# Kernel optimization log

Measured on AMD Instinct MI355X. Metric: run time of the kernel, lower is better.

The kernel has to match this reference:

```python
import jax, jax.numpy as jnp
import numpy as np

N_EMBD = 1024
N_HEAD = 16
HEAD_DIM = N_EMBD // N_HEAD
B, T = 2, 2048


def setup_inputs() -> dict:
    key = jax.random.key(0)
    k1, k2, k3 = jax.random.split(key, 3)
    s_in = 1.0 / np.sqrt(N_EMBD)
    return {
        "x": jax.random.normal(k1, (B, T, N_EMBD), dtype=jnp.float32),
        "w_qkv": jax.random.normal(k2, (N_EMBD, 3 * N_EMBD), dtype=jnp.float32) * s_in,
        "b_qkv": jnp.zeros((3 * N_EMBD,), dtype=jnp.float32),
        "w_out": jax.random.normal(k3, (N_EMBD, N_EMBD), dtype=jnp.float32) * s_in,
        "b_out": jnp.zeros((N_EMBD,), dtype=jnp.float32),
    }


def reference(x, w_qkv, b_qkv, w_out, b_out):
    b, t, c = x.shape
    qkv = x @ w_qkv + b_qkv  # [B,T,3C]
    q, k, v = jnp.split(qkv, 3, axis=-1)
    # [B,T,C] -> [B,H,T,D]
    reshape = lambda a: a.reshape(b, t, N_HEAD, HEAD_DIM).transpose(0, 2, 1, 3)
    q, k, v = reshape(q), reshape(k), reshape(v)
    scale = 1.0 / jnp.sqrt(jnp.asarray(HEAD_DIM, dtype=x.dtype))
    att = jnp.einsum("bhqd,bhkd->bhqk", q, k) * scale  # [B,H,T,T]
    causal = jnp.tril(jnp.ones((t, t), dtype=bool))
    att = jnp.where(causal, att, jnp.asarray(-jnp.inf, dtype=att.dtype))
    att = jax.nn.softmax(att, axis=-1)
    y = jnp.einsum("bhqk,bhkd->bhqd", att, v)  # [B,H,T,D]
    y = y.transpose(0, 2, 1, 3).reshape(b, t, c)
    return y @ w_out + b_out
```

## Files before the change

### kernel.cpp

```cpp
#include <hip/hip_runtime.h>

typedef unsigned short u16;
typedef __attribute__((ext_vector_type(8))) short s16x8;
typedef __attribute__((ext_vector_type(8))) unsigned short u16x8;
typedef __attribute__((ext_vector_type(4))) unsigned short u16x4;
typedef __attribute__((ext_vector_type(4))) float f32x4;

__device__ __forceinline__ u16 f2bf(float f) {
  unsigned int u = __float_as_uint(f);
  u += 0x7fffu + ((u >> 16) & 1u);
  return (u16)(u >> 16);
}

__device__ __forceinline__ void gload_lds16(const u16* g, u16* l) {
  __builtin_amdgcn_global_load_lds((__attribute__((address_space(1))) void*)(u16*)g,
                                   (__attribute__((address_space(3))) void*)l, 16, 0, 0);
}

__global__ void __launch_bounds__(256) cvt_bf16_kernel(const float* __restrict__ in,
                                                       u16* __restrict__ out) {
  int i = (blockIdx.x * 256 + threadIdx.x) * 8;
  float4 a = *(const float4*)(in + i);
  float4 b = *(const float4*)(in + i + 4);
  u16x8 o;
  o[0] = f2bf(a.x); o[1] = f2bf(a.y); o[2] = f2bf(a.z); o[3] = f2bf(a.w);
  o[4] = f2bf(b.x); o[5] = f2bf(b.y); o[6] = f2bf(b.z); o[7] = f2bf(b.w);
  *(u16x8*)(out + i) = o;
}

__global__ void __launch_bounds__(256) transpose_cvt_kernel(const float* __restrict__ in,
                                                            u16* __restrict__ out,
                                                            int K, int N) {
  __shared__ float tile[32][33];
  int n0 = blockIdx.x * 32, k0 = blockIdx.y * 32;
  int r = threadIdx.x >> 5, c = threadIdx.x & 31;
#pragma unroll
  for (int i = 0; i < 4; ++i)
    tile[r + i * 8][c] = in[(size_t)(k0 + r + i * 8) * N + n0 + c];
  __syncthreads();
#pragma unroll
  for (int i = 0; i < 4; ++i)
    out[(size_t)(n0 + r + i * 8) * K + k0 + c] = f2bf(tile[c][r + i * 8]);
}

__device__ __forceinline__ void gemm_core(const u16* __restrict__ A,
                                          const u16* __restrict__ BT, int K,
                                          int m0, int n0, u16* As, u16* Bs,
                                          f32x4 acc[4][4]) {
  const int tid = threadIdx.x;
  const int lane = tid & 63, wave = tid >> 6;
  const int quad = lane >> 4, l16 = lane & 15;
  const int wm = (wave & 1) << 6, wn = (wave >> 1) << 6;
  const int ob0 = wave * 2048 + lane * 16;
  const int ob1 = ob0 + 1024;
  const int r0 = ob0 >> 6, c0 = (ob0 & 63) >> 1;
  const int r1 = ob1 >> 6, c1 = (ob1 & 63) >> 1;

  for (int k0 = 0; k0 < K; k0 += 32) {
    __syncthreads();
    gload_lds16(&A [(size_t)(m0 + r0) * K + k0 + c0], &As[ob0 >> 1]);
    gload_lds16(&A [(size_t)(m0 + r1) * K + k0 + c1], &As[ob1 >> 1]);
    gload_lds16(&BT[(size_t)(n0 + r0) * K + k0 + c0], &Bs[ob0 >> 1]);
    gload_lds16(&BT[(size_t)(n0 + r1) * K + k0 + c1], &Bs[ob1 >> 1]);
    __syncthreads();
    s16x8 a[4], b[4];
#pragma unroll
    for (int i = 0; i < 4; ++i)
      a[i] = *(const s16x8*)&As[(wm + i * 16 + l16) * 32 + quad * 8];
#pragma unroll
    for (int j = 0; j < 4; ++j)
      b[j] = *(const s16x8*)&Bs[(wn + j * 16 + l16) * 32 + quad * 8];
#pragma unroll
    for (int i = 0; i < 4; ++i)
#pragma unroll
      for (int j = 0; j < 4; ++j)
        acc[i][j] = __builtin_amdgcn_mfma_f32_16x16x32_bf16(a[i], b[j], acc[i][j], 0, 0, 0);
  }
}

__global__ void __launch_bounds__(256) gemm_qkv_kernel(const u16* __restrict__ xbf,
                                                       const u16* __restrict__ wT,
                                                       const float* __restrict__ bias,
                                                       u16* __restrict__ qb,
                                                       u16* __restrict__ kb,
                                                       u16* __restrict__ vtb) {
  __shared__ u16 As[128 * 32], Bs[128 * 32];
  f32x4 acc[4][4];
#pragma unroll
  for (int i = 0; i < 4; ++i)
#pragma unroll
    for (int j = 0; j < 4; ++j) { f32x4 z = {0.f, 0.f, 0.f, 0.f}; acc[i][j] = z; }
  const int m0 = blockIdx.x * 128, n0 = blockIdx.y * 128;
  gemm_core(xbf, wT, 1024, m0, n0, As, Bs, acc);

  const int tid = threadIdx.x;
  const int lane = tid & 63, wave = tid >> 6;
  const int quad = lane >> 4, l16 = lane & 15;
  const int wm = (wave & 1) << 6, wn = (wave >> 1) << 6;
  const int sec = n0 >> 10;
#pragma unroll
  for (int i = 0; i < 4; ++i)
#pragma unroll
    for (int j = 0; j < 4; ++j) {
      const int gm = m0 + wm + i * 16 + quad * 4;
      const int gn = n0 + wn + j * 16 + l16;
      const float bv = bias[gn];
      const int c = gn & 1023, h = c >> 6, d = c & 63;
#pragma unroll
      for (int r = 0; r < 4; ++r) {
        const int row = gm + r;
        const int bb = row >> 11, t = row & 2047;
        if (sec == 0)      qb[((size_t)(bb * 16 + h) * 2048 + t) * 64 + d] = f2bf((acc[i][j][r] + bv) * 0.125f);
        else if (sec == 1) kb[((size_t)(bb * 16 + h) * 2048 + t) * 64 + d] = f2bf(acc[i][j][r] + bv);
        else               vtb[((size_t)(bb * 16 + h) * 64 + d) * 2048 + t] = f2bf(acc[i][j][r] + bv);
      }
    }
}

__global__ void __launch_bounds__(256) gemm_out_kernel(const u16* __restrict__ yb,
                                                       const u16* __restrict__ wT,
                                                       const float* __restrict__ bias,
                                                       float* __restrict__ out) {
  __shared__ u16 As[64 * 32], Bs[128 * 32];
  f32x4 acc[2][4];
#pragma unroll
  for (int i = 0; i < 2; ++i)
#pragma unroll
    for (int j = 0; j < 4; ++j) { f32x4 z = {0.f, 0.f, 0.f, 0.f}; acc[i][j] = z; }
  const int m0 = blockIdx.x * 64, n0 = blockIdx.y * 128;
  const int K = 1024;

  const int tid = threadIdx.x;
  const int lane = tid & 63, wave = tid >> 6;
  const int quad = lane >> 4, l16 = lane & 15;
  const int wm = (wave & 1) << 5, wn = (wave >> 1) << 6;
  const int oa = tid * 16;
  const int ra = oa >> 6, ca = (oa & 63) >> 1;
  const int ob0 = wave * 2048 + lane * 16;
  const int ob1 = ob0 + 1024;
  const int rb0 = ob0 >> 6, cb0 = (ob0 & 63) >> 1;
  const int rb1 = ob1 >> 6, cb1 = (ob1 & 63) >> 1;

  for (int k0 = 0; k0 < K; k0 += 32) {
    __syncthreads();
    gload_lds16(&yb[(size_t)(m0 + ra) * K + k0 + ca],  &As[oa >> 1]);
    gload_lds16(&wT[(size_t)(n0 + rb0) * K + k0 + cb0], &Bs[ob0 >> 1]);
    gload_lds16(&wT[(size_t)(n0 + rb1) * K + k0 + cb1], &Bs[ob1 >> 1]);
    __syncthreads();
    s16x8 a[2], b[4];
#pragma unroll
    for (int i = 0; i < 2; ++i)
      a[i] = *(const s16x8*)&As[(wm + i * 16 + l16) * 32 + quad * 8];
#pragma unroll
    for (int j = 0; j < 4; ++j)
      b[j] = *(const s16x8*)&Bs[(wn + j * 16 + l16) * 32 + quad * 8];
#pragma unroll
    for (int i = 0; i < 2; ++i)
#pragma unroll
      for (int j = 0; j < 4; ++j)
        acc[i][j] = __builtin_amdgcn_mfma_f32_16x16x32_bf16(a[i], b[j], acc[i][j], 0, 0, 0);
  }

#pragma unroll
  for (int i = 0; i < 2; ++i)
#pragma unroll
    for (int j = 0; j < 4; ++j) {
      const int gm = m0 + wm + i * 16 + quad * 4;
      const int gn = n0 + wn + j * 16 + l16;
      const float bv = bias[gn];
#pragma unroll
      for (int r = 0; r < 4; ++r)
        out[(size_t)(gm + r) * 1024 + gn] = acc[i][j][r] + bv;
    }
}

__global__ void __launch_bounds__(256) attn_kernel(const u16* __restrict__ qb,
                                                   const u16* __restrict__ kb,
                                                   const u16* __restrict__ vtb,
                                                   u16* __restrict__ yb) {
  const int KSTR = 72, VSTR = 136;
  __shared__ u16 Ks[128 * 72];
  __shared__ u16 VTs[64 * 136];
  __shared__ u16 Ps[4 * 16 * 136];

  const int qt = 31 - blockIdx.x;
  const int bh = blockIdx.y;
  const int bb = bh >> 4, h = bh & 15;
  const u16* Q  = qb  + (size_t)bh * (2048 * 64);
  const u16* Km = kb  + (size_t)bh * (2048 * 64);
  const u16* VT = vtb + (size_t)bh * (64 * 2048);

  const int tid = threadIdx.x;
  const int wave = tid >> 6, lane = tid & 63;
  const int quad = lane >> 4, l16 = lane & 15;
  const float NINF = -__builtin_inff();
  const int Kr = tid >> 3, Kc = (tid & 7) * 8;
  const int Vr = tid >> 4, Vc = (tid & 15) * 8;
  u16* Pw = Ps + wave * (16 * 136);

  const int nkt = (qt >> 1) + 1;
#pragma unroll
  for (int i = 0; i < 2; ++i) {
    int r = Kr + i * 32;
    *(u16x8*)&Ks[r * KSTR + Kc] = *(const u16x8*)&Q[(size_t)(qt * 64 + r) * 64 + Kc];
  }
  __syncthreads();
  s16x8 qf[2];
#pragma unroll
  for (int ks = 0; ks < 2; ++ks)
    qf[ks] = *(const s16x8*)&Ks[(wave * 16 + l16) * KSTR + ks * 32 + quad * 8];

  float lsum = 0.f;
  f32x4 oacc[4];
#pragma unroll
  for (int dt = 0; dt < 4; ++dt) { f32x4 z = {0.f, 0.f, 0.f, 0.f}; oacc[dt] = z; }

  u16x8 kv[4], vv[4];
#pragma unroll
  for (int i = 0; i < 4; ++i) {
    kv[i] = *(const u16x8*)&Km[(size_t)(Kr + i * 32) * 64 + Kc];
    vv[i] = *(const u16x8*)&VT[(size_t)(Vr + i * 16) * 2048 + Vc];
  }

  for (int kt = 0; kt < nkt; ++kt) {
    __syncthreads();
#pragma unroll
    for (int i = 0; i < 4; ++i) {
      *(u16x8*)&Ks[(Kr + i * 32) * KSTR + Kc]  = kv[i];
      *(u16x8*)&VTs[(Vr + i * 16) * VSTR + Vc] = vv[i];
    }
    __syncthreads();
    if (kt + 1 < nkt) {
#pragma unroll
      for (int i = 0; i < 4; ++i) {
        kv[i] = *(const u16x8*)&Km[(size_t)((kt + 1) * 128 + Kr + i * 32) * 64 + Kc];
        vv[i] = *(const u16x8*)&VT[(size_t)(Vr + i * 16) * 2048 + (kt + 1) * 128 + Vc];
      }
    }
    f32x4 st[2][4];
#pragma unroll
    for (int hh = 0; hh < 2; ++hh)
#pragma unroll
      for (int mt = 0; mt < 4; ++mt) {
        f32x4 z = {0.f, 0.f, 0.f, 0.f};
        s16x8 kf0 = *(const s16x8*)&Ks[(hh * 64 + mt * 16 + l16) * KSTR + quad * 8];
        s16x8 kf1 = *(const s16x8*)&Ks[(hh * 64 + mt * 16 + l16) * KSTR + 32 + quad * 8];
        z = __builtin_amdgcn_mfma_f32_16x16x32_bf16(kf0, qf[0], z, 0, 0, 0);
        st[hh][mt] = __builtin_amdgcn_mfma_f32_16x16x32_bf16(kf1, qf[1], z, 0, 0, 0);
      }
    if (kt == nkt - 1) {
      const int qrow = qt * 64 + wave * 16 + l16;
#pragma unroll
      for (int hh = 0; hh < 2; ++hh)
#pragma unroll
        for (int mt = 0; mt < 4; ++mt)
#pragma unroll
          for (int r = 0; r < 4; ++r) {
            int kcol = kt * 128 + hh * 64 + mt * 16 + quad * 4 + r;
            if (kcol > qrow) st[hh][mt][r] = NINF;
          }
    }
#pragma unroll
    for (int hh = 0; hh < 2; ++hh)
#pragma unroll
      for (int mt = 0; mt < 4; ++mt) {
        u16x4 pw;
#pragma unroll
        for (int r = 0; r < 4; ++r) {
          float e = __expf(st[hh][mt][r]);
          lsum += e;
          pw[r] = (u16)((__float_as_uint(e) + 0x8000u) >> 16);
        }
        *(u16x4*)&Pw[l16 * VSTR + hh * 64 + mt * 16 + quad * 4] = pw;
      }
#pragma unroll
    for (int kq = 0; kq < 4; ++kq) {
      s16x8 pf = *(const s16x8*)&Pw[l16 * VSTR + kq * 32 + quad * 8];
#pragma unroll
      for (int dt = 0; dt < 4; ++dt) {
        s16x8 vf = *(const s16x8*)&VTs[(dt * 16 + l16) * VSTR + kq * 32 + quad * 8];
        oacc[dt] = __builtin_amdgcn_mfma_f32_16x16x32_bf16(pf, vf, oacc[dt], 0, 0, 0);
      }
    }
  }

  float l = lsum;
  l += __shfl_xor(l, 16, 64);
  l += __shfl_xor(l, 32, 64);
  float rinv[4];
#pragma unroll
  for (int r = 0; r < 4; ++r) rinv[r] = 1.0f / __shfl(l, quad * 4 + r, 64);
#pragma unroll
  for (int dt = 0; dt < 4; ++dt) {
    int d = dt * 16 + l16;
#pragma unroll
    for (int r = 0; r < 4; ++r) {
      int t = qt * 64 + wave * 16 + quad * 4 + r;
      yb[(((size_t)bb * 2048 + t) * 16 + h) * 64 + d] = f2bf(oacc[dt][r] * rinv[r]);
    }
  }
}

extern "C" void kernel_launch(void* const* d_in, const int* in_sizes, int n_in,
                              void* d_out, int out_size, void* d_ws, size_t ws_size,
                              hipStream_t stream) {
  (void)in_sizes; (void)n_in; (void)out_size; (void)ws_size;
  const float* x    = (const float*)d_in[0];
  const float* wqkv = (const float*)d_in[1];
  const float* bqkv = (const float*)d_in[2];
  const float* wout = (const float*)d_in[3];
  const float* bout = (const float*)d_in[4];
  float* out = (float*)d_out;

  char* ws = (char*)d_ws;
  u16* xbf   = (u16*)(ws);
  u16* wqkvT = (u16*)(ws + (size_t)8  * 1024 * 1024);
  u16* woutT = (u16*)(ws + (size_t)14 * 1024 * 1024);
  u16* qb    = (u16*)(ws + (size_t)16 * 1024 * 1024);
  u16* kb    = (u16*)(ws + (size_t)24 * 1024 * 1024);
  u16* vtb   = (u16*)(ws + (size_t)32 * 1024 * 1024);
  u16* yb    = (u16*)(ws + (size_t)40 * 1024 * 1024);

  cvt_bf16_kernel<<<2048, 256, 0, stream>>>(x, xbf);
  transpose_cvt_kernel<<<dim3(96, 32), 256, 0, stream>>>(wqkv, wqkvT, 1024, 3072);
  transpose_cvt_kernel<<<dim3(32, 32), 256, 0, stream>>>(wout, woutT, 1024, 1024);
  gemm_qkv_kernel<<<dim3(32, 24), 256, 0, stream>>>(xbf, wqkvT, bqkv, qb, kb, vtb);
  attn_kernel<<<dim3(32, 32), 256, 0, stream>>>(qb, kb, vtb, yb);
  gemm_out_kernel<<<dim3(64, 8), 256, 0, stream>>>(yb, woutT, bout, out);
}
```

Baseline: 206.8 us.

## Double-buffer GEMM LDS tiles and pair causal query tiles per attention block

Both GEMM kernels now use two LDS buffers and issue the async global-to-LDS loads for the next K slice before computing on the current one. This drops one barrier per iteration and overlaps load latency with MFMA work. The attention kernel now gives each block two query tiles (p and 31-p), so every block does the same causal work, and launches half as many blocks. The cost is doubled LDS in the GEMMs and fewer, longer attention blocks, which may lower occupancy or parallelism.

```diff
diff --git a/kernel.cpp b/kernel.cpp
--- a/kernel.cpp
+++ b/kernel.cpp
@@ -56,20 +56,29 @@
   const int r0 = ob0 >> 6, c0 = (ob0 & 63) >> 1;
   const int r1 = ob1 >> 6, c1 = (ob1 & 63) >> 1;
 
-  for (int k0 = 0; k0 < K; k0 += 32) {
+  gload_lds16(&A [(size_t)(m0 + r0) * K + c0], &As[ob0 >> 1]);
+  gload_lds16(&A [(size_t)(m0 + r1) * K + c1], &As[ob1 >> 1]);
+  gload_lds16(&BT[(size_t)(n0 + r0) * K + c0], &Bs[ob0 >> 1]);
+  gload_lds16(&BT[(size_t)(n0 + r1) * K + c1], &Bs[ob1 >> 1]);
+
+  int buf = 0;
+  for (int k0 = 0; k0 < K; k0 += 32, buf ^= 1) {
     __syncthreads();
-    gload_lds16(&A [(size_t)(m0 + r0) * K + k0 + c0], &As[ob0 >> 1]);
-    gload_lds16(&A [(size_t)(m0 + r1) * K + k0 + c1], &As[ob1 >> 1]);
-    gload_lds16(&BT[(size_t)(n0 + r0) * K + k0 + c0], &Bs[ob0 >> 1]);
-    gload_lds16(&BT[(size_t)(n0 + r1) * K + k0 + c1], &Bs[ob1 >> 1]);
-    __syncthreads();
+    if (k0 + 32 < K) {
+      const int nb = (buf ^ 1) * (128 * 32);
+      gload_lds16(&A [(size_t)(m0 + r0) * K + k0 + 32 + c0], &As[nb + (ob0 >> 1)]);
+      gload_lds16(&A [(size_t)(m0 + r1) * K + k0 + 32 + c1], &As[nb + (ob1 >> 1)]);
+      gload_lds16(&BT[(size_t)(n0 + r0) * K + k0 + 32 + c0], &Bs[nb + (ob0 >> 1)]);
+      gload_lds16(&BT[(size_t)(n0 + r1) * K + k0 + 32 + c1], &Bs[nb + (ob1 >> 1)]);
+    }
+    const int cb = buf * (128 * 32);
     s16x8 a[4], b[4];
 #pragma unroll
     for (int i = 0; i < 4; ++i)
-      a[i] = *(const s16x8*)&As[(wm + i * 16 + l16) * 32 + quad * 8];
+      a[i] = *(const s16x8*)&As[cb + (wm + i * 16 + l16) * 32 + quad * 8];
 #pragma unroll
     for (int j = 0; j < 4; ++j)
-      b[j] = *(const s16x8*)&Bs[(wn + j * 16 + l16) * 32 + quad * 8];
+      b[j] = *(const s16x8*)&Bs[cb + (wn + j * 16 + l16) * 32 + quad * 8];
 #pragma unroll
     for (int i = 0; i < 4; ++i)
 #pragma unroll
@@ -84,7 +93,7 @@
                                                        u16* __restrict__ qb,
                                                        u16* __restrict__ kb,
                                                        u16* __restrict__ vtb) {
-  __shared__ u16 As[128 * 32], Bs[128 * 32];
+  __shared__ u16 As[2 * 128 * 32], Bs[2 * 128 * 32];
   f32x4 acc[4][4];
 #pragma unroll
   for (int i = 0; i < 4; ++i)
@@ -121,7 +130,7 @@
                                                        const u16* __restrict__ wT,
                                                        const float* __restrict__ bias,
                                                        float* __restrict__ out) {
-  __shared__ u16 As[64 * 32], Bs[128 * 32];
+  __shared__ u16 As[2 * 64 * 32], Bs[2 * 128 * 32];
   f32x4 acc[2][4];
 #pragma unroll
   for (int i = 0; i < 2; ++i)
@@ -141,19 +150,27 @@
   const int rb0 = ob0 >> 6, cb0 = (ob0 & 63) >> 1;
   const int rb1 = ob1 >> 6, cb1 = (ob1 & 63) >> 1;
 
-  for (int k0 = 0; k0 < K; k0 += 32) {
+  gload_lds16(&yb[(size_t)(m0 + ra) * K + ca],   &As[oa >> 1]);
+  gload_lds16(&wT[(size_t)(n0 + rb0) * K + cb0], &Bs[ob0 >> 1]);
+  gload_lds16(&wT[(size_t)(n0 + rb1) * K + cb1], &Bs[ob1 >> 1]);
+
+  int buf = 0;
+  for (int k0 = 0; k0 < K; k0 += 32, buf ^= 1) {
     __syncthreads();
-    gload_lds16(&yb[(size_t)(m0 + ra) * K + k0 + ca],  &As[oa >> 1]);
-    gload_lds16(&wT[(size_t)(n0 + rb0) * K + k0 + cb0], &Bs[ob0 >> 1]);
-    gload_lds16(&wT[(size_t)(n0 + rb1) * K + k0 + cb1], &Bs[ob1 >> 1]);
-    __syncthreads();
+    if (k0 + 32 < K) {
+      const int nbA = (buf ^ 1) * (64 * 32), nbB = (buf ^ 1) * (128 * 32);
+      gload_lds16(&yb[(size_t)(m0 + ra) * K + k0 + 32 + ca],   &As[nbA + (oa >> 1)]);
+      gload_lds16(&wT[(size_t)(n0 + rb0) * K + k0 + 32 + cb0], &Bs[nbB + (ob0 >> 1)]);
+      gload_lds16(&wT[(size_t)(n0 + rb1) * K + k0 + 32 + cb1], &Bs[nbB + (ob1 >> 1)]);
+    }
+    const int cbA = buf * (64 * 32), cbB = buf * (128 * 32);
     s16x8 a[2], b[4];
 #pragma unroll
     for (int i = 0; i < 2; ++i)
-      a[i] = *(const s16x8*)&As[(wm + i * 16 + l16) * 32 + quad * 8];
+      a[i] = *(const s16x8*)&As[cbA + (wm + i * 16 + l16) * 32 + quad * 8];
 #pragma unroll
     for (int j = 0; j < 4; ++j)
-      b[j] = *(const s16x8*)&Bs[(wn + j * 16 + l16) * 32 + quad * 8];
+      b[j] = *(const s16x8*)&Bs[cbB + (wn + j * 16 + l16) * 32 + quad * 8];
 #pragma unroll
     for (int i = 0; i < 2; ++i)
 #pragma unroll
@@ -183,7 +200,7 @@
   __shared__ u16 VTs[64 * 136];
   __shared__ u16 Ps[4 * 16 * 136];
 
-  const int qt = 31 - blockIdx.x;
+  const int p = blockIdx.x;
   const int bh = blockIdx.y;
   const int bb = bh >> 4, h = bh & 15;
   const u16* Q  = qb  + (size_t)bh * (2048 * 64);
@@ -198,105 +215,109 @@
   const int Vr = tid >> 4, Vc = (tid & 15) * 8;
   u16* Pw = Ps + wave * (16 * 136);
 
-  const int nkt = (qt >> 1) + 1;
-#pragma unroll
-  for (int i = 0; i < 2; ++i) {
-    int r = Kr + i * 32;
-    *(u16x8*)&Ks[r * KSTR + Kc] = *(const u16x8*)&Q[(size_t)(qt * 64 + r) * 64 + Kc];
-  }
-  __syncthreads();
-  s16x8 qf[2];
-#pragma unroll
-  for (int ks = 0; ks < 2; ++ks)
-    qf[ks] = *(const s16x8*)&Ks[(wave * 16 + l16) * KSTR + ks * 32 + quad * 8];
-
-  float lsum = 0.f;
-  f32x4 oacc[4];
-#pragma unroll
-  for (int dt = 0; dt < 4; ++dt) { f32x4 z = {0.f, 0.f, 0.f, 0.f}; oacc[dt] = z; }
-
-  u16x8 kv[4], vv[4];
-#pragma unroll
-  for (int i = 0; i < 4; ++i) {
-    kv[i] = *(const u16x8*)&Km[(size_t)(Kr + i * 32) * 64 + Kc];
-    vv[i] = *(const u16x8*)&VT[(size_t)(Vr + i * 16) * 2048 + Vc];
-  }
-
-  for (int kt = 0; kt < nkt; ++kt) {
+  for (int pass = 0; pass < 2; ++pass) {
+    const int qt = pass ? (31 - p) : p;
+    const int nkt = (qt >> 1) + 1;
     __syncthreads();
 #pragma unroll
+    for (int i = 0; i < 2; ++i) {
+      int r = Kr + i * 32;
+      *(u16x8*)&Ks[r * KSTR + Kc] = *(const u16x8*)&Q[(size_t)(qt * 64 + r) * 64 + Kc];
+    }
+    __syncthreads();
+    s16x8 qf[2];
+#pragma unroll
+    for (int ks = 0; ks < 2; ++ks)
+      qf[ks] = *(const s16x8*)&Ks[(wave * 16 + l16) * KSTR + ks * 32 + quad * 8];
+
+    float lsum = 0.f;
+    f32x4 oacc[4];
+#pragma unroll
+    for (int dt = 0; dt < 4; ++dt) { f32x4 z = {0.f, 0.f, 0.f, 0.f}; oacc[dt] = z; }
+
+    u16x8 kv[4], vv[4];
+#pragma unroll
     for (int i = 0; i < 4; ++i) {
-      *(u16x8*)&Ks[(Kr + i * 32) * KSTR + Kc]  = kv[i];
-      *(u16x8*)&VTs[(Vr + i * 16) * VSTR + Vc] = vv[i];
-    }
-    __syncthreads();
-    if (kt + 1 < nkt) {
+      kv[i] = *(const u16x8*)&Km[(size_t)(Kr + i * 32) * 64 + Kc];
+      vv[i] = *(const u16x8*)&VT[(size_t)(Vr + i * 16) * 2048 + Vc];
+    }
+
+    for (int kt = 0; kt < nkt; ++kt) {
+      __syncthreads();
 #pragma unroll
       for (int i = 0; i < 4; ++i) {
-        kv[i] = *(const u16x8*)&Km[(size_t)((kt + 1) * 128 + Kr + i * 32) * 64 + Kc];
-        vv[i] = *(const u16x8*)&VT[(size_t)(Vr + i * 16) * 2048 + (kt + 1) * 128 + Vc];
-      }
-    }
-    f32x4 st[2][4];
-#pragma unroll
-    for (int hh = 0; hh < 2; ++hh)
-#pragma unroll
-      for (int mt = 0; mt < 4; ++mt) {
-        f32x4 z = {0.f, 0.f, 0.f, 0.f};
-        s16x8 kf0 = *(const s16x8*)&Ks[(hh * 64 + mt * 16 + l16) * KSTR + quad * 8];
-        s16x8 kf1 = *(const s16x8*)&Ks[(hh * 64 + mt * 16 + l16) * KSTR + 32 + quad * 8];
-        z = __builtin_amdgcn_mfma_f32_16x16x32_bf16(kf0, qf[0], z, 0, 0, 0);
-        st[hh][mt] = __builtin_amdgcn_mfma_f32_16x16x32_bf16(kf1, qf[1], z, 0, 0, 0);
-      }
-    if (kt == nkt - 1) {
-      const int qrow = qt * 64 + wave * 16 + l16;
+        *(u16x8*)&Ks[(Kr + i * 32) * KSTR + Kc]  = kv[i];
+        *(u16x8*)&VTs[(Vr + i * 16) * VSTR + Vc] = vv[i];
+      }
+      __syncthreads();
+      if (kt + 1 < nkt) {
+#pragma unroll
+        for (int i = 0; i < 4; ++i) {
+          kv[i] = *(const u16x8*)&Km[(size_t)((kt + 1) * 128 + Kr + i * 32) * 64 + Kc];
+          vv[i] = *(const u16x8*)&VT[(size_t)(Vr + i * 16) * 2048 + (kt + 1) * 128 + Vc];
+        }
+      }
+      f32x4 st[2][4];
 #pragma unroll
       for (int hh = 0; hh < 2; ++hh)
 #pragma unroll
-        for (int mt = 0; mt < 4; ++mt)
+        for (int mt = 0; mt < 4; ++mt) {
+          f32x4 z = {0.f, 0.f, 0.f, 0.f};
+          s16x8 kf0 = *(const s16x8*)&Ks[(hh * 64 + mt * 16 + l16) * KSTR + quad * 8];
+          s16x8 kf1 = *(const s16x8*)&Ks[(hh * 64 + mt * 16 + l16) * KSTR + 32 + quad * 8];
+          z = __builtin_amdgcn_mfma_f32_16x16x32_bf16(kf0, qf[0], z, 0, 0, 0);
+          st[hh][mt] = __builtin_amdgcn_mfma_f32_16x16x32_bf16(kf1, qf[1], z, 0, 0, 0);
+        }
+      if (kt == nkt - 1) {
+        const int qrow = qt * 64 + wave * 16 + l16;
+#pragma unroll
+        for (int hh = 0; hh < 2; ++hh)
+#pragma unroll
+          for (int mt = 0; mt < 4; ++mt)
+#pragma unroll
+            for (int r = 0; r < 4; ++r) {
+              int kcol = kt * 128 + hh * 64 + mt * 16 + quad * 4 + r;
+              if (kcol > qrow) st[hh][mt][r] = NINF;
+            }
+      }
+#pragma unroll
+      for (int hh = 0; hh < 2; ++hh)
+#pragma unroll
+        for (int mt = 0; mt < 4; ++mt) {
+          u16x4 pw;
 #pragma unroll
           for (int r = 0; r < 4; ++r) {
-            int kcol = kt * 128 + hh * 64 + mt * 16 + quad * 4 + r;
-            if (kcol > qrow) st[hh][mt][r] = NINF;
+            float e = __expf(st[hh][mt][r]);
+            lsum += e;
+            pw[r] = (u16)((__float_as_uint(e) + 0x8000u) >> 16);
           }
-    }
-#pragma unroll
-    for (int hh = 0; hh < 2; ++hh)
-#pragma unroll
-      for (int mt = 0; mt < 4; ++mt) {
-        u16x4 pw;
-#pragma unroll
-        for (int r = 0; r < 4; ++r) {
-          float e = __expf(st[hh][mt][r]);
-          lsum += e;
-          pw[r] = (u16)((__float_as_uint(e) + 0x8000u) >> 16);
+          *(u16x4*)&Pw[l16 * VSTR + hh * 64 + mt * 16 + quad * 4] = pw;
         }
-        *(u16x4*)&Pw[l16 * VSTR + hh * 64 + mt * 16 + quad * 4] = pw;
-      }
-#pragma unroll
-    for (int kq = 0; kq < 4; ++kq) {
-      s16x8 pf = *(const s16x8*)&Pw[l16 * VSTR + kq * 32 + quad * 8];
-#pragma unroll
-      for (int dt = 0; dt < 4; ++dt) {
-        s16x8 vf = *(const s16x8*)&VTs[(dt * 16 + l16) * VSTR + kq * 32 + quad * 8];
-        oacc[dt] = __builtin_amdgcn_mfma_f32_16x16x32_bf16(pf, vf, oacc[dt], 0, 0, 0);
-      }
-    }
-  }
-
-  float l = lsum;
-  l += __shfl_xor(l, 16, 64);
-  l += __shfl_xor(l, 32, 64);
-  float rinv[4];
-#pragma unroll
-  for (int r = 0; r < 4; ++r) rinv[r] = 1.0f / __shfl(l, quad * 4 + r, 64);
-#pragma unroll
-  for (int dt = 0; dt < 4; ++dt) {
-    int d = dt * 16 + l16;
-#pragma unroll
-    for (int r = 0; r < 4; ++r) {
-      int t = qt * 64 + wave * 16 + quad * 4 + r;
-      yb[(((size_t)bb * 2048 + t) * 16 + h) * 64 + d] = f2bf(oacc[dt][r] * rinv[r]);
+#pragma unroll
+      for (int kq = 0; kq < 4; ++kq) {
+        s16x8 pf = *(const s16x8*)&Pw[l16 * VSTR + kq * 32 + quad * 8];
+#pragma unroll
+        for (int dt = 0; dt < 4; ++dt) {
+          s16x8 vf = *(const s16x8*)&VTs[(dt * 16 + l16) * VSTR + kq * 32 + quad * 8];
+          oacc[dt] = __builtin_amdgcn_mfma_f32_16x16x32_bf16(pf, vf, oacc[dt], 0, 0, 0);
+        }
+      }
+    }
+
+    float l = lsum;
+    l += __shfl_xor(l, 16, 64);
+    l += __shfl_xor(l, 32, 64);
+    float rinv[4];
+#pragma unroll
+    for (int r = 0; r < 4; ++r) rinv[r] = 1.0f / __shfl(l, quad * 4 + r, 64);
+#pragma unroll
+    for (int dt = 0; dt < 4; ++dt) {
+      int d = dt * 16 + l16;
+#pragma unroll
+      for (int r = 0; r < 4; ++r) {
+        int t = qt * 64 + wave * 16 + quad * 4 + r;
+        yb[(((size_t)bb * 2048 + t) * 16 + h) * 64 + d] = f2bf(oacc[dt][r] * rinv[r]);
+      }
     }
   }
 }
@@ -325,6 +346,6 @@
   transpose_cvt_kernel<<<dim3(96, 32), 256, 0, stream>>>(wqkv, wqkvT, 1024, 3072);
   transpose_cvt_kernel<<<dim3(32, 32), 256, 0, stream>>>(wout, woutT, 1024, 1024);
   gemm_qkv_kernel<<<dim3(32, 24), 256, 0, stream>>>(xbf, wqkvT, bqkv, qb, kb, vtb);
-  attn_kernel<<<dim3(32, 32), 256, 0, stream>>>(qb, kb, vtb, yb);
+  attn_kernel<<<dim3(16, 32), 256, 0, stream>>>(qb, kb, vtb, yb);
   gemm_out_kernel<<<dim3(64, 8), 256, 0, stream>>>(yb, woutT, bout, out);
 }
```

Result: faster. 196.7 us (-4.9%).

## Pair causal query tiles per attention block and merge prep kernels into one launch

Applied to the files above, without the earlier changes.

Each attention block now handles two query tiles, p and 31-p, so every block gets the same causal work. Each K/V tile staged in LDS is reused by both query tiles, and the grid is halved. The three conversion and transpose launches are also merged into one prep kernel to cut launch overhead. The cost is more live registers (two sets of accumulators and Q fragments) and fewer blocks, which may lower occupancy.

```diff
diff --git a/kernel.cpp b/kernel.cpp
--- a/kernel.cpp
+++ b/kernel.cpp
@@ -17,23 +17,29 @@
                                    (__attribute__((address_space(3))) void*)l, 16, 0, 0);
 }
 
-__global__ void __launch_bounds__(256) cvt_bf16_kernel(const float* __restrict__ in,
-                                                       u16* __restrict__ out) {
-  int i = (blockIdx.x * 256 + threadIdx.x) * 8;
-  float4 a = *(const float4*)(in + i);
-  float4 b = *(const float4*)(in + i + 4);
-  u16x8 o;
-  o[0] = f2bf(a.x); o[1] = f2bf(a.y); o[2] = f2bf(a.z); o[3] = f2bf(a.w);
-  o[4] = f2bf(b.x); o[5] = f2bf(b.y); o[6] = f2bf(b.z); o[7] = f2bf(b.w);
-  *(u16x8*)(out + i) = o;
-}
-
-__global__ void __launch_bounds__(256) transpose_cvt_kernel(const float* __restrict__ in,
-                                                            u16* __restrict__ out,
-                                                            int K, int N) {
+__global__ void __launch_bounds__(256) prep_kernel(const float* __restrict__ x,
+                                                   u16* __restrict__ xbf,
+                                                   const float* __restrict__ wqkv,
+                                                   u16* __restrict__ wqkvT,
+                                                   const float* __restrict__ wout,
+                                                   u16* __restrict__ woutT) {
   __shared__ float tile[32][33];
-  int n0 = blockIdx.x * 32, k0 = blockIdx.y * 32;
-  int r = threadIdx.x >> 5, c = threadIdx.x & 31;
+  const int b = blockIdx.x, tid = threadIdx.x;
+  if (b < 2048) {
+    int i = (b * 256 + tid) * 8;
+    float4 a = *(const float4*)(x + i);
+    float4 c = *(const float4*)(x + i + 4);
+    u16x8 o;
+    o[0] = f2bf(a.x); o[1] = f2bf(a.y); o[2] = f2bf(a.z); o[3] = f2bf(a.w);
+    o[4] = f2bf(c.x); o[5] = f2bf(c.y); o[6] = f2bf(c.z); o[7] = f2bf(c.w);
+    *(u16x8*)(xbf + i) = o;
+    return;
+  }
+  const float* in; u16* out; int K = 1024, N, bx, by;
+  if (b < 5120) { in = wqkv; out = wqkvT; N = 3072; bx = (b - 2048) % 96; by = (b - 2048) / 96; }
+  else          { in = wout; out = woutT; N = 1024; bx = (b - 5120) % 32; by = (b - 5120) / 32; }
+  int n0 = bx * 32, k0 = by * 32;
+  int r = tid >> 5, c = tid & 31;
 #pragma unroll
   for (int i = 0; i < 4; ++i)
     tile[r + i * 8][c] = in[(size_t)(k0 + r + i * 8) * N + n0 + c];
@@ -183,7 +189,7 @@
   __shared__ u16 VTs[64 * 136];
   __shared__ u16 Ps[4 * 16 * 136];
 
-  const int qt = 31 - blockIdx.x;
+  const int p = blockIdx.x;
   const int bh = blockIdx.y;
   const int bb = bh >> 4, h = bh & 15;
   const u16* Q  = qb  + (size_t)bh * (2048 * 64);
@@ -198,22 +204,37 @@
   const int Vr = tid >> 4, Vc = (tid & 15) * 8;
   u16* Pw = Ps + wave * (16 * 136);
 
-  const int nkt = (qt >> 1) + 1;
+  const int qtA = p, qtB = 31 - p;
+  const int nktA = (qtA >> 1) + 1, nktB = (qtB >> 1) + 1;
+
+  s16x8 qfA[2], qfB[2];
 #pragma unroll
   for (int i = 0; i < 2; ++i) {
     int r = Kr + i * 32;
-    *(u16x8*)&Ks[r * KSTR + Kc] = *(const u16x8*)&Q[(size_t)(qt * 64 + r) * 64 + Kc];
+    *(u16x8*)&Ks[r * KSTR + Kc] = *(const u16x8*)&Q[(size_t)(qtA * 64 + r) * 64 + Kc];
   }
   __syncthreads();
-  s16x8 qf[2];
 #pragma unroll
   for (int ks = 0; ks < 2; ++ks)
-    qf[ks] = *(const s16x8*)&Ks[(wave * 16 + l16) * KSTR + ks * 32 + quad * 8];
-
-  float lsum = 0.f;
-  f32x4 oacc[4];
-#pragma unroll
-  for (int dt = 0; dt < 4; ++dt) { f32x4 z = {0.f, 0.f, 0.f, 0.f}; oacc[dt] = z; }
+    qfA[ks] = *(const s16x8*)&Ks[(wave * 16 + l16) * KSTR + ks * 32 + quad * 8];
+  __syncthreads();
+#pragma unroll
+  for (int i = 0; i < 2; ++i) {
+    int r = Kr + i * 32;
+    *(u16x8*)&Ks[r * KSTR + Kc] = *(const u16x8*)&Q[(size_t)(qtB * 64 + r) * 64 + Kc];
+  }
+  __syncthreads();
+#pragma unroll
+  for (int ks = 0; ks < 2; ++ks)
+    qfB[ks] = *(const s16x8*)&Ks[(wave * 16 + l16) * KSTR + ks * 32 + quad * 8];
+
+  float lsumA = 0.f, lsumB = 0.f;
+  f32x4 oaccA[4], oaccB[4];
+#pragma unroll
+  for (int dt = 0; dt < 4; ++dt) {
+    f32x4 z = {0.f, 0.f, 0.f, 0.f};
+    oaccA[dt] = z; oaccB[dt] = z;
+  }
 
   u16x8 kv[4], vv[4];
 #pragma unroll
@@ -222,21 +243,8 @@
     vv[i] = *(const u16x8*)&VT[(size_t)(Vr + i * 16) * 2048 + Vc];
   }
 
-  for (int kt = 0; kt < nkt; ++kt) {
-    __syncthreads();
-#pragma unroll
-    for (int i = 0; i < 4; ++i) {
-      *(u16x8*)&Ks[(Kr + i * 32) * KSTR + Kc]  = kv[i];
-      *(u16x8*)&VTs[(Vr + i * 16) * VSTR + Vc] = vv[i];
-    }
-    __syncthreads();
-    if (kt + 1 < nkt) {
-#pragma unroll
-      for (int i = 0; i < 4; ++i) {
-        kv[i] = *(const u16x8*)&Km[(size_t)((kt + 1) * 128 + Kr + i * 32) * 64 + Kc];
-        vv[i] = *(const u16x8*)&VT[(size_t)(Vr + i * 16) * 2048 + (kt + 1) * 128 + Vc];
-      }
-    }
+  auto do_tile = [&](const s16x8 qf[2], int qt, int nkt, int kt,
+                     float& lsum, f32x4 oacc[4]) {
     f32x4 st[2][4];
 #pragma unroll
     for (int hh = 0; hh < 2; ++hh)
@@ -282,21 +290,45 @@
         oacc[dt] = __builtin_amdgcn_mfma_f32_16x16x32_bf16(pf, vf, oacc[dt], 0, 0, 0);
       }
     }
-  }
-
-  float l = lsum;
-  l += __shfl_xor(l, 16, 64);
-  l += __shfl_xor(l, 32, 64);
-  float rinv[4];
-#pragma unroll
-  for (int r = 0; r < 4; ++r) rinv[r] = 1.0f / __shfl(l, quad * 4 + r, 64);
-#pragma unroll
-  for (int dt = 0; dt < 4; ++dt) {
-    int d = dt * 16 + l16;
-#pragma unroll
-    for (int r = 0; r < 4; ++r) {
-      int t = qt * 64 + wave * 16 + quad * 4 + r;
-      yb[(((size_t)bb * 2048 + t) * 16 + h) * 64 + d] = f2bf(oacc[dt][r] * rinv[r]);
+  };
+
+  for (int kt = 0; kt < nktB; ++kt) {
+    __syncthreads();
+#pragma unroll
+    for (int i = 0; i < 4; ++i) {
+      *(u16x8*)&Ks[(Kr + i * 32) * KSTR + Kc]  = kv[i];
+      *(u16x8*)&VTs[(Vr + i * 16) * VSTR + Vc] = vv[i];
+    }
+    __syncthreads();
+    if (kt + 1 < nktB) {
+#pragma unroll
+      for (int i = 0; i < 4; ++i) {
+        kv[i] = *(const u16x8*)&Km[(size_t)((kt + 1) * 128 + Kr + i * 32) * 64 + Kc];
+        vv[i] = *(const u16x8*)&VT[(size_t)(Vr + i * 16) * 2048 + (kt + 1) * 128 + Vc];
+      }
+    }
+    do_tile(qfB, qtB, nktB, kt, lsumB, oaccB);
+    if (kt < nktA) do_tile(qfA, qtA, nktA, kt, lsumA, oaccA);
+  }
+
+#pragma unroll
+  for (int e = 0; e < 2; ++e) {
+    const int qt = e ? qtB : qtA;
+    float l = e ? lsumB : lsumA;
+    f32x4* oacc = e ? oaccB : oaccA;
+    l += __shfl_xor(l, 16, 64);
+    l += __shfl_xor(l, 32, 64);
+    float rinv[4];
+#pragma unroll
+    for (int r = 0; r < 4; ++r) rinv[r] = 1.0f / __shfl(l, quad * 4 + r, 64);
+#pragma unroll
+    for (int dt = 0; dt < 4; ++dt) {
+      int d = dt * 16 + l16;
+#pragma unroll
+      for (int r = 0; r < 4; ++r) {
+        int t = qt * 64 + wave * 16 + quad * 4 + r;
+        yb[(((size_t)bb * 2048 + t) * 16 + h) * 64 + d] = f2bf(oacc[dt][r] * rinv[r]);
+      }
     }
   }
 }
@@ -321,10 +353,8 @@
   u16* vtb   = (u16*)(ws + (size_t)32 * 1024 * 1024);
   u16* yb    = (u16*)(ws + (size_t)40 * 1024 * 1024);
 
-  cvt_bf16_kernel<<<2048, 256, 0, stream>>>(x, xbf);
-  transpose_cvt_kernel<<<dim3(96, 32), 256, 0, stream>>>(wqkv, wqkvT, 1024, 3072);
-  transpose_cvt_kernel<<<dim3(32, 32), 256, 0, stream>>>(wout, woutT, 1024, 1024);
+  prep_kernel<<<6144, 256, 0, stream>>>(x, xbf, wqkv, wqkvT, wout, woutT);
   gemm_qkv_kernel<<<dim3(32, 24), 256, 0, stream>>>(xbf, wqkvT, bqkv, qb, kb, vtb);
-  attn_kernel<<<dim3(32, 32), 256, 0, stream>>>(qb, kb, vtb, yb);
+  attn_kernel<<<dim3(16, 32), 256, 0, stream>>>(qb, kb, vtb, yb);
   gemm_out_kernel<<<dim3(64, 8), 256, 0, stream>>>(yb, woutT, bout, out);
 }
```

After: 195.0 us. 5.7% less time.

## Fuse prep kernels and pair causal query tiles per attention block with XCD mapping

Applied to the files above, without the earlier changes.

The three conversion/transpose kernels are merged into one launch that dispatches on block index, removing two kernel launches. The attention kernel now has each block process two query tiles (p and 31-p), so every block does the same amount of causal work and the load is balanced. Block ids are remapped so that blocks sharing a batch-head land on the same XCD, which should improve L2 reuse of K/V. The cost is half as many attention blocks, which lowers parallelism, and the passes inside each block run one after the other.

```diff
diff --git a/kernel.cpp b/kernel.cpp
--- a/kernel.cpp
+++ b/kernel.cpp
@@ -17,23 +17,29 @@
                                    (__attribute__((address_space(3))) void*)l, 16, 0, 0);
 }
 
-__global__ void __launch_bounds__(256) cvt_bf16_kernel(const float* __restrict__ in,
-                                                       u16* __restrict__ out) {
-  int i = (blockIdx.x * 256 + threadIdx.x) * 8;
-  float4 a = *(const float4*)(in + i);
-  float4 b = *(const float4*)(in + i + 4);
-  u16x8 o;
-  o[0] = f2bf(a.x); o[1] = f2bf(a.y); o[2] = f2bf(a.z); o[3] = f2bf(a.w);
-  o[4] = f2bf(b.x); o[5] = f2bf(b.y); o[6] = f2bf(b.z); o[7] = f2bf(b.w);
-  *(u16x8*)(out + i) = o;
-}
-
-__global__ void __launch_bounds__(256) transpose_cvt_kernel(const float* __restrict__ in,
-                                                            u16* __restrict__ out,
-                                                            int K, int N) {
+__global__ void __launch_bounds__(256) prep_kernel(const float* __restrict__ x,
+                                                   u16* __restrict__ xbf,
+                                                   const float* __restrict__ wqkv,
+                                                   u16* __restrict__ wqkvT,
+                                                   const float* __restrict__ wout,
+                                                   u16* __restrict__ woutT) {
   __shared__ float tile[32][33];
-  int n0 = blockIdx.x * 32, k0 = blockIdx.y * 32;
-  int r = threadIdx.x >> 5, c = threadIdx.x & 31;
+  const int b = blockIdx.x, tid = threadIdx.x;
+  if (b < 2048) {
+    int i = (b * 256 + tid) * 8;
+    float4 a = *(const float4*)(x + i);
+    float4 c = *(const float4*)(x + i + 4);
+    u16x8 o;
+    o[0] = f2bf(a.x); o[1] = f2bf(a.y); o[2] = f2bf(a.z); o[3] = f2bf(a.w);
+    o[4] = f2bf(c.x); o[5] = f2bf(c.y); o[6] = f2bf(c.z); o[7] = f2bf(c.w);
+    *(u16x8*)(xbf + i) = o;
+    return;
+  }
+  const float* in; u16* out; int K = 1024, N, bx, by;
+  if (b < 5120) { in = wqkv; out = wqkvT; N = 3072; bx = (b - 2048) % 96; by = (b - 2048) / 96; }
+  else          { in = wout; out = woutT; N = 1024; bx = (b - 5120) % 32; by = (b - 5120) / 32; }
+  int n0 = bx * 32, k0 = by * 32;
+  int r = tid >> 5, c = tid & 31;
 #pragma unroll
   for (int i = 0; i < 4; ++i)
     tile[r + i * 8][c] = in[(size_t)(k0 + r + i * 8) * N + n0 + c];
@@ -183,8 +189,10 @@
   __shared__ u16 VTs[64 * 136];
   __shared__ u16 Ps[4 * 16 * 136];
 
-  const int qt = 31 - blockIdx.x;
-  const int bh = blockIdx.y;
+  const int lid = blockIdx.y * 16 + blockIdx.x;
+  const int xcd = lid & 7, idx = lid >> 3;
+  const int bh = (xcd << 2) | (idx >> 4);
+  const int p  = idx & 15;
   const int bb = bh >> 4, h = bh & 15;
   const u16* Q  = qb  + (size_t)bh * (2048 * 64);
   const u16* Km = kb  + (size_t)bh * (2048 * 64);
@@ -198,105 +206,109 @@
   const int Vr = tid >> 4, Vc = (tid & 15) * 8;
   u16* Pw = Ps + wave * (16 * 136);
 
-  const int nkt = (qt >> 1) + 1;
-#pragma unroll
-  for (int i = 0; i < 2; ++i) {
-    int r = Kr + i * 32;
-    *(u16x8*)&Ks[r * KSTR + Kc] = *(const u16x8*)&Q[(size_t)(qt * 64 + r) * 64 + Kc];
-  }
-  __syncthreads();
-  s16x8 qf[2];
-#pragma unroll
-  for (int ks = 0; ks < 2; ++ks)
-    qf[ks] = *(const s16x8*)&Ks[(wave * 16 + l16) * KSTR + ks * 32 + quad * 8];
-
-  float lsum = 0.f;
-  f32x4 oacc[4];
-#pragma unroll
-  for (int dt = 0; dt < 4; ++dt) { f32x4 z = {0.f, 0.f, 0.f, 0.f}; oacc[dt] = z; }
-
-  u16x8 kv[4], vv[4];
-#pragma unroll
-  for (int i = 0; i < 4; ++i) {
-    kv[i] = *(const u16x8*)&Km[(size_t)(Kr + i * 32) * 64 + Kc];
-    vv[i] = *(const u16x8*)&VT[(size_t)(Vr + i * 16) * 2048 + Vc];
-  }
-
-  for (int kt = 0; kt < nkt; ++kt) {
-    __syncthreads();
+  for (int pass = 0; pass < 2; ++pass) {
+    const int qt = pass ? (31 - p) : p;
+    const int nkt = (qt >> 1) + 1;
+    __syncthreads();
+#pragma unroll
+    for (int i = 0; i < 2; ++i) {
+      int r = Kr + i * 32;
+      *(u16x8*)&Ks[r * KSTR + Kc] = *(const u16x8*)&Q[(size_t)(qt * 64 + r) * 64 + Kc];
+    }
+    __syncthreads();
+    s16x8 qf[2];
+#pragma unroll
+    for (int ks = 0; ks < 2; ++ks)
+      qf[ks] = *(const s16x8*)&Ks[(wave * 16 + l16) * KSTR + ks * 32 + quad * 8];
+
+    float lsum = 0.f;
+    f32x4 oacc[4];
+#pragma unroll
+    for (int dt = 0; dt < 4; ++dt) { f32x4 z = {0.f, 0.f, 0.f, 0.f}; oacc[dt] = z; }
+
+    u16x8 kv[4], vv[4];
 #pragma unroll
     for (int i = 0; i < 4; ++i) {
-      *(u16x8*)&Ks[(Kr + i * 32) * KSTR + Kc]  = kv[i];
-      *(u16x8*)&VTs[(Vr + i * 16) * VSTR + Vc] = vv[i];
-    }
-    __syncthreads();
-    if (kt + 1 < nkt) {
+      kv[i] = *(const u16x8*)&Km[(size_t)(Kr + i * 32) * 64 + Kc];
+      vv[i] = *(const u16x8*)&VT[(size_t)(Vr + i * 16) * 2048 + Vc];
+    }
+
+    for (int kt = 0; kt < nkt; ++kt) {
+      __syncthreads();
 #pragma unroll
       for (int i = 0; i < 4; ++i) {
-        kv[i] = *(const u16x8*)&Km[(size_t)((kt + 1) * 128 + Kr + i * 32) * 64 + Kc];
-        vv[i] = *(const u16x8*)&VT[(size_t)(Vr + i * 16) * 2048 + (kt + 1) * 128 + Vc];
-      }
-    }
-    f32x4 st[2][4];
-#pragma unroll
-    for (int hh = 0; hh < 2; ++hh)
-#pragma unroll
-      for (int mt = 0; mt < 4; ++mt) {
-        f32x4 z = {0.f, 0.f, 0.f, 0.f};
-        s16x8 kf0 = *(const s16x8*)&Ks[(hh * 64 + mt * 16 + l16) * KSTR + quad * 8];
-        s16x8 kf1 = *(const s16x8*)&Ks[(hh * 64 + mt * 16 + l16) * KSTR + 32 + quad * 8];
-        z = __builtin_amdgcn_mfma_f32_16x16x32_bf16(kf0, qf[0], z, 0, 0, 0);
-        st[hh][mt] = __builtin_amdgcn_mfma_f32_16x16x32_bf16(kf1, qf[1], z, 0, 0, 0);
-      }
-    if (kt == nkt - 1) {
-      const int qrow = qt * 64 + wave * 16 + l16;
+        *(u16x8*)&Ks[(Kr + i * 32) * KSTR + Kc]  = kv[i];
+        *(u16x8*)&VTs[(Vr + i * 16) * VSTR + Vc] = vv[i];
+      }
+      __syncthreads();
+      if (kt + 1 < nkt) {
+#pragma unroll
+        for (int i = 0; i < 4; ++i) {
+          kv[i] = *(const u16x8*)&Km[(size_t)((kt + 1) * 128 + Kr + i * 32) * 64 + Kc];
+          vv[i] = *(const u16x8*)&VT[(size_t)(Vr + i * 16) * 2048 + (kt + 1) * 128 + Vc];
+        }
+      }
+      f32x4 st[2][4];
 #pragma unroll
       for (int hh = 0; hh < 2; ++hh)
 #pragma unroll
-        for (int mt = 0; mt < 4; ++mt)
+        for (int mt = 0; mt < 4; ++mt) {
+          f32x4 z = {0.f, 0.f, 0.f, 0.f};
+          s16x8 kf0 = *(const s16x8*)&Ks[(hh * 64 + mt * 16 + l16) * KSTR + quad * 8];
+          s16x8 kf1 = *(const s16x8*)&Ks[(hh * 64 + mt * 16 + l16) * KSTR + 32 + quad * 8];
+          z = __builtin_amdgcn_mfma_f32_16x16x32_bf16(kf0, qf[0], z, 0, 0, 0);
+          st[hh][mt] = __builtin_amdgcn_mfma_f32_16x16x32_bf16(kf1, qf[1], z, 0, 0, 0);
+        }
+      if (kt == nkt - 1) {
+        const int qrow = qt * 64 + wave * 16 + l16;
+#pragma unroll
+        for (int hh = 0; hh < 2; ++hh)
+#pragma unroll
+          for (int mt = 0; mt < 4; ++mt)
+#pragma unroll
+            for (int r = 0; r < 4; ++r) {
+              int kcol = kt * 128 + hh * 64 + mt * 16 + quad * 4 + r;
+              if (kcol > qrow) st[hh][mt][r] = NINF;
+            }
+      }
+#pragma unroll
+      for (int hh = 0; hh < 2; ++hh)
+#pragma unroll
+        for (int mt = 0; mt < 4; ++mt) {
+          u16x4 pw;
 #pragma unroll
           for (int r = 0; r < 4; ++r) {
-            int kcol = kt * 128 + hh * 64 + mt * 16 + quad * 4 + r;
-            if (kcol > qrow) st[hh][mt][r] = NINF;
+            float e = __expf(st[hh][mt][r]);
+            lsum += e;
+            pw[r] = (u16)((__float_as_uint(e) + 0x8000u) >> 16);
           }
-    }
-#pragma unroll
-    for (int hh = 0; hh < 2; ++hh)
-#pragma unroll
-      for (int mt = 0; mt < 4; ++mt) {
-        u16x4 pw;
-#pragma unroll
-        for (int r = 0; r < 4; ++r) {
-          float e = __expf(st[hh][mt][r]);
-          lsum += e;
-          pw[r] = (u16)((__float_as_uint(e) + 0x8000u) >> 16);
+          *(u16x4*)&Pw[l16 * VSTR + hh * 64 + mt * 16 + quad * 4] = pw;
         }
-        *(u16x4*)&Pw[l16 * VSTR + hh * 64 + mt * 16 + quad * 4] = pw;
-      }
-#pragma unroll
-    for (int kq = 0; kq < 4; ++kq) {
-      s16x8 pf = *(const s16x8*)&Pw[l16 * VSTR + kq * 32 + quad * 8];
-#pragma unroll
-      for (int dt = 0; dt < 4; ++dt) {
-        s16x8 vf = *(const s16x8*)&VTs[(dt * 16 + l16) * VSTR + kq * 32 + quad * 8];
-        oacc[dt] = __builtin_amdgcn_mfma_f32_16x16x32_bf16(pf, vf, oacc[dt], 0, 0, 0);
-      }
-    }
-  }
-
-  float l = lsum;
-  l += __shfl_xor(l, 16, 64);
-  l += __shfl_xor(l, 32, 64);
-  float rinv[4];
-#pragma unroll
-  for (int r = 0; r < 4; ++r) rinv[r] = 1.0f / __shfl(l, quad * 4 + r, 64);
-#pragma unroll
-  for (int dt = 0; dt < 4; ++dt) {
-    int d = dt * 16 + l16;
-#pragma unroll
-    for (int r = 0; r < 4; ++r) {
-      int t = qt * 64 + wave * 16 + quad * 4 + r;
-      yb[(((size_t)bb * 2048 + t) * 16 + h) * 64 + d] = f2bf(oacc[dt][r] * rinv[r]);
+#pragma unroll
+      for (int kq = 0; kq < 4; ++kq) {
+        s16x8 pf = *(const s16x8*)&Pw[l16 * VSTR + kq * 32 + quad * 8];
+#pragma unroll
+        for (int dt = 0; dt < 4; ++dt) {
+          s16x8 vf = *(const s16x8*)&VTs[(dt * 16 + l16) * VSTR + kq * 32 + quad * 8];
+          oacc[dt] = __builtin_amdgcn_mfma_f32_16x16x32_bf16(pf, vf, oacc[dt], 0, 0, 0);
+        }
+      }
+    }
+
+    float l = lsum;
+    l += __shfl_xor(l, 16, 64);
+    l += __shfl_xor(l, 32, 64);
+    float rinv[4];
+#pragma unroll
+    for (int r = 0; r < 4; ++r) rinv[r] = 1.0f / __shfl(l, quad * 4 + r, 64);
+#pragma unroll
+    for (int dt = 0; dt < 4; ++dt) {
+      int d = dt * 16 + l16;
+#pragma unroll
+      for (int r = 0; r < 4; ++r) {
+        int t = qt * 64 + wave * 16 + quad * 4 + r;
+        yb[(((size_t)bb * 2048 + t) * 16 + h) * 64 + d] = f2bf(oacc[dt][r] * rinv[r]);
+      }
     }
   }
 }
@@ -321,10 +333,8 @@
   u16* vtb   = (u16*)(ws + (size_t)32 * 1024 * 1024);
   u16* yb    = (u16*)(ws + (size_t)40 * 1024 * 1024);
 
-  cvt_bf16_kernel<<<2048, 256, 0, stream>>>(x, xbf);
-  transpose_cvt_kernel<<<dim3(96, 32), 256, 0, stream>>>(wqkv, wqkvT, 1024, 3072);
-  transpose_cvt_kernel<<<dim3(32, 32), 256, 0, stream>>>(wout, woutT, 1024, 1024);
+  prep_kernel<<<6144, 256, 0, stream>>>(x, xbf, wqkv, wqkvT, wout, woutT);
   gemm_qkv_kernel<<<dim3(32, 24), 256, 0, stream>>>(xbf, wqkvT, bqkv, qb, kb, vtb);
-  attn_kernel<<<dim3(32, 32), 256, 0, stream>>>(qb, kb, vtb, yb);
+  attn_kernel<<<dim3(16, 32), 256, 0, stream>>>(qb, kb, vtb, yb);
   gemm_out_kernel<<<dim3(64, 8), 256, 0, stream>>>(yb, woutT, bout, out);
 }
```

Result: faster. 179.5 us (-13.2%).
